# Kernel tuning notes

Measured on AMD Instinct MI355X. Metric: run time of the kernel, lower is better.

Reference implementation:

```python
import jax, jax.numpy as jnp
import numpy as np

B, T, C = 4, 2048, 2048  # batch, n_target, n_context
KEY_SIZE = 1024
VALUE_SIZE = 1024
NUM_HEADS = 16
KEY_HIDDEN = 64
HEAD_SIZE = VALUE_SIZE // NUM_HEADS  # 64
NORMALISE = True


def setup_inputs() -> dict:
    key = jax.random.key(0)
    ks = jax.random.split(key, 7)
    s = 0.02
    return {
        "queries": jax.random.normal(ks[0], (B, T, KEY_SIZE), jnp.float32),
        "keys": jax.random.normal(ks[1], (B, C, KEY_SIZE), jnp.float32),
        "values": jax.random.normal(ks[2], (B, C, VALUE_SIZE), jnp.float32),
        "Wq": jax.random.normal(ks[3], (NUM_HEADS * KEY_HIDDEN, KEY_SIZE), jnp.float32) * s,
        "Wk": jax.random.normal(ks[4], (NUM_HEADS * KEY_HIDDEN, KEY_SIZE), jnp.float32) * s,
        "Wv": jax.random.normal(ks[5], (NUM_HEADS * HEAD_SIZE, VALUE_SIZE), jnp.float32) * s,
        "Wo": jax.random.normal(ks[6], (VALUE_SIZE, NUM_HEADS * HEAD_SIZE), jnp.float32) * s,
    }


def reference(queries, keys, values, Wq, Wk, Wv, Wo):
    # Linear projections (torch nn.Linear: x @ W.T), reshape to heads
    q = (queries @ Wq.T).reshape(B, T, NUM_HEADS, KEY_HIDDEN)   # [B,T,H,Dk]
    k = (keys @ Wk.T).reshape(B, C, NUM_HEADS, KEY_HIDDEN)      # [B,C,H,Dk]
    v = (values @ Wv.T).reshape(B, C, NUM_HEADS, HEAD_SIZE)     # [B,C,H,Dv]
    scale = np.sqrt(KEY_HIDDEN).astype(np.float32)
    # Scores [B,H,T,C]
    scores = jnp.einsum('bthd,bchd->bhtc', q, k) / scale
    if NORMALISE:
        attn = jax.nn.softmax(scores, axis=-1)
    else:
        attn = jax.nn.sigmoid(scores)
    out = jnp.einsum('bhtc,bchd->bthd', attn, v)                # [B,T,H,Dv]
    out = out.reshape(B, T, NUM_HEADS * HEAD_SIZE)
    return out @ Wo.T                                            # [B,T,VALUE_SIZE]
```

## Files before the change

kernel.cpp:

```cpp
#include <hip/hip_runtime.h>
#include <stdint.h>

#define BATCH 4
#define SEQ   2048
#define EMB   1024
#define NH    16
#define HD    64

typedef __attribute__((ext_vector_type(4))) float  floatx4;
typedef __attribute__((ext_vector_type(8))) short  shortx8;

__device__ __forceinline__ unsigned short f2bf(float f) {
  unsigned u = __builtin_bit_cast(unsigned, f);
  u += 0x7FFFu + ((u >> 16) & 1u);
  return (unsigned short)(u >> 16);
}

__device__ __forceinline__ unsigned pack2bf(float a, float b) {
  return (unsigned)f2bf(a) | ((unsigned)f2bf(b) << 16);
}

__device__ __forceinline__ unsigned packtrunc(float a, float b) {
#if __has_builtin(__builtin_amdgcn_perm)
  return __builtin_amdgcn_perm(__builtin_bit_cast(unsigned, b),
                               __builtin_bit_cast(unsigned, a), 0x07060302u);
#else
  return (__builtin_bit_cast(unsigned, a) >> 16) |
         (__builtin_bit_cast(unsigned, b) & 0xFFFF0000u);
#endif
}

__device__ __forceinline__ float fexp2(float x) {
#if __has_builtin(__builtin_amdgcn_exp2f)
  return __builtin_amdgcn_exp2f(x);
#else
  return exp2f(x);
#endif
}

__device__ __forceinline__ void gl_lds16(const void* g, void* l) {
  __builtin_amdgcn_global_load_lds((const __attribute__((address_space(1))) void*)g,
                                   (__attribute__((address_space(3))) void*)l,
                                   16, 0, 0);
}

__device__ __forceinline__ void cast_body(const float* __restrict__ in,
                                          unsigned short* __restrict__ out, int bb, int t) {
  size_t i = (size_t)bb * 256 + t;
  const float4* p = (const float4*)in + i * 2;
  float4 f0 = p[0], f1 = p[1];
  uint4 o;
  o.x = pack2bf(f0.x, f0.y);
  o.y = pack2bf(f0.z, f0.w);
  o.z = pack2bf(f1.x, f1.y);
  o.w = pack2bf(f1.z, f1.w);
  ((uint4*)out)[i] = o;
}

__global__ __launch_bounds__(256) void cast_bf16(const float* __restrict__ in,
                                                 unsigned short* __restrict__ out) {
  cast_body(in, out, blockIdx.x, threadIdx.x);
}

__global__ __launch_bounds__(256) void cast_all(
    const float* __restrict__ q, const float* __restrict__ k, const float* __restrict__ v,
    const float* __restrict__ w0, const float* __restrict__ w1,
    const float* __restrict__ w2, const float* __restrict__ w3,
    unsigned short* __restrict__ oq, unsigned short* __restrict__ ok, unsigned short* __restrict__ ov,
    unsigned short* __restrict__ ow0, unsigned short* __restrict__ ow1,
    unsigned short* __restrict__ ow2, unsigned short* __restrict__ ow3) {
  int bb = blockIdx.x;
  const float* in; unsigned short* out;
  if      (bb < 4096)  { in = q;  out = oq; }
  else if (bb < 8192)  { in = k;  out = ok;  bb -= 4096; }
  else if (bb < 12288) { in = v;  out = ov;  bb -= 8192; }
  else if (bb < 12800) { in = w0; out = ow0; bb -= 12288; }
  else if (bb < 13312) { in = w1; out = ow1; bb -= 12800; }
  else if (bb < 13824) { in = w2; out = ow2; bb -= 13312; }
  else                 { in = w3; out = ow3; bb -= 13824; }
  cast_body(in, out, bb, threadIdx.x);
}

__global__ __launch_bounds__(256) void cast_w4(const float* __restrict__ i0, const float* __restrict__ i1,
                                               const float* __restrict__ i2, const float* __restrict__ i3,
                                               unsigned short* __restrict__ o0, unsigned short* __restrict__ o1,
                                               unsigned short* __restrict__ o2, unsigned short* __restrict__ o3) {
  int bb = blockIdx.x;
  const float* in; unsigned short* out;
  if      (bb < 512)  { in = i0; out = o0; }
  else if (bb < 1024) { in = i1; out = o1; bb -= 512; }
  else if (bb < 1536) { in = i2; out = o2; bb -= 1024; }
  else                { in = i3; out = o3; bb -= 1536; }
  cast_body(in, out, bb, threadIdx.x);
}

template <bool CF32>
__device__ __forceinline__ void gemm_body(const unsigned short* __restrict__ A,
                                          const unsigned short* __restrict__ Bt,
                                          void* __restrict__ Cp, float cscale) {
  constexpr int N = EMB, K = EMB;
  constexpr int BM = 128, BN = 128, BK = 64;
  __shared__ unsigned short As[BM * BK];
  __shared__ unsigned short Bs[BN * BK];
  const int t = threadIdx.x, w = t >> 6, lane = t & 63;
  const int quad = lane >> 4, lrow = lane & 15;
  const int m0 = blockIdx.y * BM, n0 = blockIdx.x * BN;
  const int wm = (w >> 1) * 64, wn = (w & 1) * 64;
  floatx4 acc[4][4] = {};

  const unsigned short* asrc[4];
  const unsigned short* bsrc[4];
#pragma unroll
  for (int i = 0; i < 4; i++) {
    int q = i * 256 + t;
    int r = q >> 3, kc = (q & 7) ^ (r & 7);
    asrc[i] = A + (size_t)(m0 + r) * K + kc * 8;
    bsrc[i] = Bt + (size_t)(n0 + r) * K + kc * 8;
  }

  for (int k0 = 0; k0 < K; k0 += BK) {
#pragma unroll
    for (int i = 0; i < 4; i++) {
      gl_lds16(asrc[i], (char*)As + (size_t)(i * 256 + w * 64) * 16);
      gl_lds16(bsrc[i], (char*)Bs + (size_t)(i * 256 + w * 64) * 16);
      asrc[i] += BK; bsrc[i] += BK;
    }
    __syncthreads();
#pragma unroll
    for (int ks = 0; ks < 2; ks++) {
      shortx8 a[4];
#pragma unroll
      for (int mi = 0; mi < 4; mi++) {
        int row = wm + mi * 16 + lrow;
        a[mi] = *(const shortx8*)(As + row * 64 + (((ks * 4 + quad) ^ (row & 7)) * 8));
      }
#pragma unroll
      for (int ni = 0; ni < 4; ni++) {
        int rowb = wn + ni * 16 + lrow;
        shortx8 b = *(const shortx8*)(Bs + rowb * 64 + (((ks * 4 + quad) ^ (rowb & 7)) * 8));
#pragma unroll
        for (int mi = 0; mi < 4; mi++)
          acc[mi][ni] = __builtin_amdgcn_mfma_f32_16x16x32_bf16(a[mi], b, acc[mi][ni], 0, 0, 0);
      }
    }
    __syncthreads();
  }
#pragma unroll
  for (int mi = 0; mi < 4; mi++)
#pragma unroll
    for (int ni = 0; ni < 4; ni++)
#pragma unroll
      for (int r = 0; r < 4; r++) {
        int row = m0 + wm + mi * 16 + quad * 4 + r;
        int col = n0 + wn + ni * 16 + lrow;
        float v = acc[mi][ni][r] * cscale;
        if constexpr (CF32) ((float*)Cp)[(size_t)row * N + col] = v;
        else                ((unsigned short*)Cp)[(size_t)row * N + col] = f2bf(v);
      }
}

__global__ __launch_bounds__(256, 2) void gemm_qkv(
    const unsigned short* __restrict__ Xq, const unsigned short* __restrict__ Xk,
    const unsigned short* __restrict__ Xv,
    const unsigned short* __restrict__ Wq, const unsigned short* __restrict__ Wk,
    const unsigned short* __restrict__ Wv,
    unsigned short* __restrict__ Oq, unsigned short* __restrict__ Ok,
    unsigned short* __restrict__ Ov, float sq) {
  const unsigned short *A, *Bt; unsigned short* C; float sc;
  if (blockIdx.z == 0)      { A = Xq; Bt = Wq; C = Oq; sc = sq; }
  else if (blockIdx.z == 1) { A = Xk; Bt = Wk; C = Ok; sc = 1.0f; }
  else                      { A = Xv; Bt = Wv; C = Ov; sc = 1.0f; }
  gemm_body<false>(A, Bt, C, sc);
}

__global__ __launch_bounds__(256, 2) void gemm_o(const unsigned short* __restrict__ A,
                                                 const unsigned short* __restrict__ Bt,
                                                 float* __restrict__ C) {
  gemm_body<true>(A, Bt, C, 1.0f);
}

__global__ __launch_bounds__(256) void transpose_v(const unsigned short* __restrict__ vp,
                                                   unsigned short* __restrict__ vT) {
  __shared__ unsigned short tile[64][72];
  const int c0 = blockIdx.x * 64, h = blockIdx.y, b = blockIdx.z;
  const int t = threadIdx.x;
#pragma unroll
  for (int i = 0; i < 2; i++) {
    int q = t + 256 * i;
    int r = q >> 3, dc = (q & 7) * 8;
    uint4 v = *(const uint4*)(vp + ((size_t)(b * SEQ + c0 + r)) * EMB + h * HD + dc);
    *(uint4*)&tile[r][dc] = v;
  }
  __syncthreads();
#pragma unroll
  for (int i = 0; i < 2; i++) {
    int q = t + 256 * i;
    int d = q >> 3, a = q & 7;
    unsigned e[8];
#pragma unroll
    for (int u = 0; u < 8; u++) {
      int cp = 8 * a + u;
      int c = 32 * (cp >> 5) + 16 * (cp & 1) + ((cp & 31) >> 1);
      e[u] = tile[c][d];
    }
    uint4 o;
    o.x = e[0] | (e[1] << 16); o.y = e[2] | (e[3] << 16);
    o.z = e[4] | (e[5] << 16); o.w = e[6] | (e[7] << 16);
    *(uint4*)(vT + ((size_t)((b * NH + h) * HD + d)) * SEQ + c0 + 8 * a) = o;
  }
}

__global__ __launch_bounds__(256, 3) void flash_attn(const unsigned short* __restrict__ qp,
                                                     const unsigned short* __restrict__ kp,
                                                     const unsigned short* __restrict__ vT,
                                                     unsigned short* __restrict__ ao) {
  __shared__ unsigned short Qs[128 * 64];
  __shared__ unsigned short Ks[2][64 * 64];
  __shared__ unsigned short Vts[2][64 * 64];
  __shared__ unsigned short Ps[4][16 * 40];
  const int t0 = blockIdx.x * 128, h = blockIdx.y, b = blockIdx.z;
  const int t = threadIdx.x, w = t >> 6, lane = t & 63;
  const int quad = lane >> 4, lrow = lane & 15;

#pragma unroll
  for (int i = 0; i < 4; i++) {
    int p = i * 256 + t;
    int r = p >> 3, kc = (p & 7) ^ (r & 7);
    gl_lds16(qp + ((size_t)(b * SEQ + t0 + r)) * EMB + h * HD + kc * 8,
             (char*)Qs + (size_t)(i * 256 + w * 64) * 16);
  }

  const unsigned short* ksrc[2];
  const unsigned short* vsrc[2];
#pragma unroll
  for (int i = 0; i < 2; i++) {
    int p = i * 256 + t;
    int r = p >> 3, kc = (p & 7) ^ (r & 7);
    ksrc[i] = kp + ((size_t)(b * SEQ + r)) * EMB + h * HD + kc * 8;
    vsrc[i] = vT + ((size_t)((b * NH + h) * HD + r)) * SEQ + kc * 8;
  }

#pragma unroll
  for (int i = 0; i < 2; i++) {
    gl_lds16(ksrc[i], (char*)Ks[0] + (size_t)(i * 256 + w * 64) * 16);
    gl_lds16(vsrc[i], (char*)Vts[0] + (size_t)(i * 256 + w * 64) * 16);
    ksrc[i] += 64 * EMB;
    vsrc[i] += 64;
  }

  float l_st[2][4] = {};
  floatx4 accO[2][4] = {};

  for (int it = 0; it < SEQ / 64; it++) {
    const int cur = it & 1;
    __syncthreads();
    if (it + 1 < SEQ / 64) {
#pragma unroll
      for (int i = 0; i < 2; i++) {
        gl_lds16(ksrc[i], (char*)Ks[cur ^ 1] + (size_t)(i * 256 + w * 64) * 16);
        gl_lds16(vsrc[i], (char*)Vts[cur ^ 1] + (size_t)(i * 256 + w * 64) * 16);
        ksrc[i] += 64 * EMB;
        vsrc[i] += 64;
      }
    }
    const unsigned short* Kc = Ks[cur];
    const unsigned short* Vc = Vts[cur];

    floatx4 accS[2][4] = {};
#pragma unroll
    for (int kk = 0; kk < 2; kk++) {
      int qk = quad + kk * 4;
      shortx8 afr[2];
#pragma unroll
      for (int mi = 0; mi < 2; mi++) {
        int row = w * 32 + mi * 16 + lrow;
        afr[mi] = *(const shortx8*)(Qs + row * 64 + ((qk ^ (row & 7)) * 8));
      }
#pragma unroll
      for (int ni = 0; ni < 4; ni++) {
        int rowb = ni * 16 + lrow;
        shortx8 bfr = *(const shortx8*)(Kc + rowb * 64 + ((qk ^ (rowb & 7)) * 8));
#pragma unroll
        for (int mi = 0; mi < 2; mi++)
          accS[mi][ni] = __builtin_amdgcn_mfma_f32_16x16x32_bf16(afr[mi], bfr, accS[mi][ni], 0, 0, 0);
      }
    }

#pragma unroll
    for (int hh = 0; hh < 2; hh++) {
      shortx8 pafr[2];
#pragma unroll
      for (int mi = 0; mi < 2; mi++) {
#pragma unroll
        for (int r = 0; r < 4; r++) {
          float p0 = fexp2(accS[mi][2 * hh][r]);
          float p1 = fexp2(accS[mi][2 * hh + 1][r]);
          l_st[mi][r] += p0 + p1;
          *(unsigned*)(&Ps[w][(quad * 4 + r) * 40 + lrow * 2]) = packtrunc(p0, p1);
        }
        pafr[mi] = *(const shortx8*)(&Ps[w][lrow * 40 + quad * 8]);
      }
#pragma unroll
      for (int nio = 0; nio < 4; nio++) {
        int d = nio * 16 + lrow;
        shortx8 bfr = *(const shortx8*)(Vc + d * 64 + ((((hh << 2) + quad) ^ (d & 7)) * 8));
#pragma unroll
        for (int mi = 0; mi < 2; mi++)
          accO[mi][nio] = __builtin_amdgcn_mfma_f32_16x16x32_bf16(pafr[mi], bfr, accO[mi][nio], 0, 0, 0);
      }
    }
  }

#pragma unroll
  for (int mi = 0; mi < 2; mi++)
#pragma unroll
    for (int r = 0; r < 4; r++) {
      float l = l_st[mi][r];
      l += __shfl_xor(l, 1);
      l += __shfl_xor(l, 2);
      l += __shfl_xor(l, 4);
      l += __shfl_xor(l, 8);
      float inv = 1.0f / l;
#pragma unroll
      for (int nio = 0; nio < 4; nio++) accO[mi][nio][r] *= inv;
    }
#pragma unroll
  for (int mi = 0; mi < 2; mi++)
#pragma unroll
    for (int nio = 0; nio < 4; nio++)
#pragma unroll
      for (int r = 0; r < 4; r++) {
        int row = t0 + w * 32 + mi * 16 + quad * 4 + r;
        int col = h * HD + nio * 16 + lrow;
        ao[((size_t)(b * SEQ + row)) * EMB + col] = f2bf(accO[mi][nio][r]);
      }
}

extern "C" void kernel_launch(void* const* d_in, const int* in_sizes, int n_in,
                              void* d_out, int out_size, void* d_ws, size_t ws_size,
                              hipStream_t stream) {
  const float* queries = (const float*)d_in[0];
  const float* keys    = (const float*)d_in[1];
  const float* values  = (const float*)d_in[2];
  const float* Wq      = (const float*)d_in[3];
  const float* Wk      = (const float*)d_in[4];
  const float* Wv      = (const float*)d_in[5];
  const float* Wo      = (const float*)d_in[6];

  char* ws = (char*)d_ws;
  const size_t MB = 1ull << 20;
  const float SC2 = 0.125f * 1.44269504088896341f;

  unsigned short* wq_b = (unsigned short*)(ws + 0 * MB);
  unsigned short* wk_b = (unsigned short*)(ws + 2 * MB);
  unsigned short* wv_b = (unsigned short*)(ws + 4 * MB);
  unsigned short* wo_b = (unsigned short*)(ws + 6 * MB);

  dim3 gg(EMB / 128, (BATCH * SEQ) / 128);

  if (ws_size >= 104 * MB) {
    unsigned short* Xq = (unsigned short*)(ws + 8 * MB);
    unsigned short* Xk = (unsigned short*)(ws + 24 * MB);
    unsigned short* Xv = (unsigned short*)(ws + 40 * MB);
    unsigned short* qp = (unsigned short*)(ws + 56 * MB);
    unsigned short* kp = (unsigned short*)(ws + 72 * MB);
    unsigned short* vp = (unsigned short*)(ws + 88 * MB);
    unsigned short* vT = Xk;
    unsigned short* ao = Xq;

    cast_all<<<14336, 256, 0, stream>>>(queries, keys, values, Wq, Wk, Wv, Wo,
                                        Xq, Xk, Xv, wq_b, wk_b, wv_b, wo_b);
    gemm_qkv<<<dim3(gg.x, gg.y, 3), 256, 0, stream>>>(Xq, Xk, Xv, wq_b, wk_b, wv_b,
                                                      qp, kp, vp, SC2);
    transpose_v<<<dim3(SEQ / 64, NH, BATCH), 256, 0, stream>>>(vp, vT);
    flash_attn<<<dim3(SEQ / 128, NH, BATCH), 256, 0, stream>>>(qp, kp, vT, ao);
    gemm_o<<<gg, 256, 0, stream>>>(ao, wo_b, (float*)d_out);
  } else {
    unsigned short* X  = (unsigned short*)(ws + 8 * MB);
    unsigned short* qp = (unsigned short*)(ws + 24 * MB);
    unsigned short* kp = (unsigned short*)(ws + 40 * MB);
    unsigned short* vp = (unsigned short*)(ws + 56 * MB);
    unsigned short* vT = (unsigned short*)(ws + 72 * MB);
    unsigned short* ao = X;

    cast_w4<<<2048, 256, 0, stream>>>(Wq, Wk, Wv, Wo, wq_b, wk_b, wv_b, wo_b);
    cast_bf16<<<4096, 256, 0, stream>>>(queries, X);
    gemm_qkv<<<dim3(gg.x, gg.y, 1), 256, 0, stream>>>(X, X, X, wq_b, wq_b, wq_b,
                                                      qp, qp, qp, SC2);
    cast_bf16<<<4096, 256, 0, stream>>>(keys, X);
    gemm_qkv<<<dim3(gg.x, gg.y, 1), 256, 0, stream>>>(X, X, X, wk_b, wk_b, wk_b,
                                                      kp, kp, kp, 1.0f);
    cast_bf16<<<4096, 256, 0, stream>>>(values, X);
    gemm_qkv<<<dim3(gg.x, gg.y, 1), 256, 0, stream>>>(X, X, X, wv_b, wv_b, wv_b,
                                                      vp, vp, vp, 1.0f);
    transpose_v<<<dim3(SEQ / 64, NH, BATCH), 256, 0, stream>>>(vp, vT);
    flash_attn<<<dim3(SEQ / 128, NH, BATCH), 256, 0, stream>>>(qp, kp, vT, ao);
    gemm_o<<<gg, 256, 0, stream>>>(ao, wo_b, (float*)d_out);
  }
}
```

Before: 349.7 us.

## Fuse V transpose into QKV GEMM epilogue and single-buffer flash attention tiles

The V projection GEMM now writes its output already transposed into the head-major vT layout through an LDS staging tile, so the separate transpose_v kernel and its round trip through global memory go away. Flash attention drops its K/V double buffering in favour of a single buffer with a sync on each side of the load, and raises its launch bound to 4 blocks per CU. The gemm_qkv kernel now reserves an extra ~34KB LDS transpose tile on every block (even the Q/K ones), which may lower GEMM occupancy. The attention loop also loses the overlap between loading the next tile and computing the current one, and relies on higher occupancy to hide that latency instead.

```diff
diff --git a/kernel.cpp b/kernel.cpp
--- a/kernel.cpp
+++ b/kernel.cpp
@@ -94,14 +94,15 @@
   cast_body(in, out, bb, threadIdx.x);
 }
 
-template <bool CF32>
+#define TST 136
+template <int MODE>
 __device__ __forceinline__ void gemm_body(const unsigned short* __restrict__ A,
                                           const unsigned short* __restrict__ Bt,
-                                          void* __restrict__ Cp, float cscale) {
+                                          void* __restrict__ Cp, float cscale,
+                                          unsigned short* As, unsigned short* Bs,
+                                          unsigned short* Ts) {
   constexpr int N = EMB, K = EMB;
   constexpr int BM = 128, BN = 128, BK = 64;
-  __shared__ unsigned short As[BM * BK];
-  __shared__ unsigned short Bs[BN * BK];
   const int t = threadIdx.x, w = t >> 6, lane = t & 63;
   const int quad = lane >> 4, lrow = lane & 15;
   const int m0 = blockIdx.y * BM, n0 = blockIdx.x * BN;
@@ -145,18 +146,46 @@
     }
     __syncthreads();
   }
-#pragma unroll
-  for (int mi = 0; mi < 4; mi++)
-#pragma unroll
-    for (int ni = 0; ni < 4; ni++)
-#pragma unroll
-      for (int r = 0; r < 4; r++) {
-        int row = m0 + wm + mi * 16 + quad * 4 + r;
-        int col = n0 + wn + ni * 16 + lrow;
-        float v = acc[mi][ni][r] * cscale;
-        if constexpr (CF32) ((float*)Cp)[(size_t)row * N + col] = v;
-        else                ((unsigned short*)Cp)[(size_t)row * N + col] = f2bf(v);
-      }
+
+  if constexpr (MODE == 2) {
+#pragma unroll
+    for (int u = 0; u < 2; u++)
+#pragma unroll
+      for (int ni = 0; ni < 4; ni++) {
+        uint4 p;
+        p.x = pack2bf(acc[2 * u][ni][0], acc[2 * u + 1][ni][0]);
+        p.y = pack2bf(acc[2 * u][ni][1], acc[2 * u + 1][ni][1]);
+        p.z = pack2bf(acc[2 * u][ni][2], acc[2 * u + 1][ni][2]);
+        p.w = pack2bf(acc[2 * u][ni][3], acc[2 * u + 1][ni][3]);
+        int col = wn + ni * 16 + lrow;
+        int cloc = wm + u * 32 + quad * 8;
+        *(uint4*)(Ts + col * TST + cloc) = p;
+      }
+    __syncthreads();
+    unsigned short* vTout = (unsigned short*)Cp;
+    const int b = m0 >> 11, cbase = m0 & 2047, h0 = n0 >> 6;
+#pragma unroll
+    for (int i = 0; i < 8; i++) {
+      int g = t + 256 * i;
+      int hh2 = g >> 10, d = (g >> 4) & 63, a = g & 15;
+      uint4 v = *(const uint4*)(Ts + (hh2 * 64 + d) * TST + a * 8);
+      *(uint4*)(vTout + ((size_t)((b * NH + h0 + hh2) * HD + d)) * SEQ + cbase + a * 8) = v;
+    }
+    __syncthreads();
+  } else {
+#pragma unroll
+    for (int mi = 0; mi < 4; mi++)
+#pragma unroll
+      for (int ni = 0; ni < 4; ni++)
+#pragma unroll
+        for (int r = 0; r < 4; r++) {
+          int row = m0 + wm + mi * 16 + quad * 4 + r;
+          int col = n0 + wn + ni * 16 + lrow;
+          float v = acc[mi][ni][r] * cscale;
+          if constexpr (MODE == 1) ((float*)Cp)[(size_t)row * N + col] = v;
+          else                     ((unsigned short*)Cp)[(size_t)row * N + col] = f2bf(v);
+        }
+  }
 }
 
 __global__ __launch_bounds__(256, 2) void gemm_qkv(
@@ -165,58 +194,45 @@
     const unsigned short* __restrict__ Wq, const unsigned short* __restrict__ Wk,
     const unsigned short* __restrict__ Wv,
     unsigned short* __restrict__ Oq, unsigned short* __restrict__ Ok,
-    unsigned short* __restrict__ Ov, float sq) {
-  const unsigned short *A, *Bt; unsigned short* C; float sc;
-  if (blockIdx.z == 0)      { A = Xq; Bt = Wq; C = Oq; sc = sq; }
-  else if (blockIdx.z == 1) { A = Xk; Bt = Wk; C = Ok; sc = 1.0f; }
-  else                      { A = Xv; Bt = Wv; C = Ov; sc = 1.0f; }
-  gemm_body<false>(A, Bt, C, sc);
-}
-
+    unsigned short* __restrict__ OvT, float sq) {
+  __shared__ unsigned short As[128 * 64];
+  __shared__ unsigned short Bs[128 * 64];
+  __shared__ unsigned short Ts[128 * TST];
+  if (blockIdx.z == 0)      gemm_body<0>(Xq, Wq, Oq, sq,   As, Bs, Ts);
+  else if (blockIdx.z == 1) gemm_body<0>(Xk, Wk, Ok, 1.0f, As, Bs, Ts);
+  else                      gemm_body<2>(Xv, Wv, OvT, 1.0f, As, Bs, Ts);
+}
+
+__global__ __launch_bounds__(256, 2) void gemm_b(const unsigned short* __restrict__ A,
+                                                 const unsigned short* __restrict__ Bt,
+                                                 unsigned short* __restrict__ C, float sc) {
+  __shared__ unsigned short As[128 * 64];
+  __shared__ unsigned short Bs[128 * 64];
+  gemm_body<0>(A, Bt, C, sc, As, Bs, nullptr);
+}
+__global__ __launch_bounds__(256, 2) void gemm_vt(const unsigned short* __restrict__ A,
+                                                  const unsigned short* __restrict__ Bt,
+                                                  unsigned short* __restrict__ C) {
+  __shared__ unsigned short As[128 * 64];
+  __shared__ unsigned short Bs[128 * 64];
+  __shared__ unsigned short Ts[128 * TST];
+  gemm_body<2>(A, Bt, C, 1.0f, As, Bs, Ts);
+}
 __global__ __launch_bounds__(256, 2) void gemm_o(const unsigned short* __restrict__ A,
                                                  const unsigned short* __restrict__ Bt,
                                                  float* __restrict__ C) {
-  gemm_body<true>(A, Bt, C, 1.0f);
-}
-
-__global__ __launch_bounds__(256) void transpose_v(const unsigned short* __restrict__ vp,
-                                                   unsigned short* __restrict__ vT) {
-  __shared__ unsigned short tile[64][72];
-  const int c0 = blockIdx.x * 64, h = blockIdx.y, b = blockIdx.z;
-  const int t = threadIdx.x;
-#pragma unroll
-  for (int i = 0; i < 2; i++) {
-    int q = t + 256 * i;
-    int r = q >> 3, dc = (q & 7) * 8;
-    uint4 v = *(const uint4*)(vp + ((size_t)(b * SEQ + c0 + r)) * EMB + h * HD + dc);
-    *(uint4*)&tile[r][dc] = v;
-  }
-  __syncthreads();
-#pragma unroll
-  for (int i = 0; i < 2; i++) {
-    int q = t + 256 * i;
-    int d = q >> 3, a = q & 7;
-    unsigned e[8];
-#pragma unroll
-    for (int u = 0; u < 8; u++) {
-      int cp = 8 * a + u;
-      int c = 32 * (cp >> 5) + 16 * (cp & 1) + ((cp & 31) >> 1);
-      e[u] = tile[c][d];
-    }
-    uint4 o;
-    o.x = e[0] | (e[1] << 16); o.y = e[2] | (e[3] << 16);
-    o.z = e[4] | (e[5] << 16); o.w = e[6] | (e[7] << 16);
-    *(uint4*)(vT + ((size_t)((b * NH + h) * HD + d)) * SEQ + c0 + 8 * a) = o;
-  }
-}
-
-__global__ __launch_bounds__(256, 3) void flash_attn(const unsigned short* __restrict__ qp,
+  __shared__ unsigned short As[128 * 64];
+  __shared__ unsigned short Bs[128 * 64];
+  gemm_body<1>(A, Bt, C, 1.0f, As, Bs, nullptr);
+}
+
+__global__ __launch_bounds__(256, 4) void flash_attn(const unsigned short* __restrict__ qp,
                                                      const unsigned short* __restrict__ kp,
                                                      const unsigned short* __restrict__ vT,
                                                      unsigned short* __restrict__ ao) {
   __shared__ unsigned short Qs[128 * 64];
-  __shared__ unsigned short Ks[2][64 * 64];
-  __shared__ unsigned short Vts[2][64 * 64];
+  __shared__ unsigned short Ks[64 * 64];
+  __shared__ unsigned short Vts[64 * 64];
   __shared__ unsigned short Ps[4][16 * 40];
   const int t0 = blockIdx.x * 128, h = blockIdx.y, b = blockIdx.z;
   const int t = threadIdx.x, w = t >> 6, lane = t & 63;
@@ -240,31 +256,19 @@
     vsrc[i] = vT + ((size_t)((b * NH + h) * HD + r)) * SEQ + kc * 8;
   }
 
-#pragma unroll
-  for (int i = 0; i < 2; i++) {
-    gl_lds16(ksrc[i], (char*)Ks[0] + (size_t)(i * 256 + w * 64) * 16);
-    gl_lds16(vsrc[i], (char*)Vts[0] + (size_t)(i * 256 + w * 64) * 16);
-    ksrc[i] += 64 * EMB;
-    vsrc[i] += 64;
-  }
-
   float l_st[2][4] = {};
   floatx4 accO[2][4] = {};
 
-  for (int it = 0; it < SEQ / 64; it++) {
-    const int cur = it & 1;
-    __syncthreads();
-    if (it + 1 < SEQ / 64) {
-#pragma unroll
-      for (int i = 0; i < 2; i++) {
-        gl_lds16(ksrc[i], (char*)Ks[cur ^ 1] + (size_t)(i * 256 + w * 64) * 16);
-        gl_lds16(vsrc[i], (char*)Vts[cur ^ 1] + (size_t)(i * 256 + w * 64) * 16);
-        ksrc[i] += 64 * EMB;
-        vsrc[i] += 64;
-      }
-    }
-    const unsigned short* Kc = Ks[cur];
-    const unsigned short* Vc = Vts[cur];
+  for (int c0 = 0; c0 < SEQ; c0 += 64) {
+    __syncthreads();
+#pragma unroll
+    for (int i = 0; i < 2; i++) {
+      gl_lds16(ksrc[i], (char*)Ks + (size_t)(i * 256 + w * 64) * 16);
+      gl_lds16(vsrc[i], (char*)Vts + (size_t)(i * 256 + w * 64) * 16);
+      ksrc[i] += 64 * EMB;
+      vsrc[i] += 64;
+    }
+    __syncthreads();
 
     floatx4 accS[2][4] = {};
 #pragma unroll
@@ -279,7 +283,7 @@
 #pragma unroll
       for (int ni = 0; ni < 4; ni++) {
         int rowb = ni * 16 + lrow;
-        shortx8 bfr = *(const shortx8*)(Kc + rowb * 64 + ((qk ^ (rowb & 7)) * 8));
+        shortx8 bfr = *(const shortx8*)(Ks + rowb * 64 + ((qk ^ (rowb & 7)) * 8));
 #pragma unroll
         for (int mi = 0; mi < 2; mi++)
           accS[mi][ni] = __builtin_amdgcn_mfma_f32_16x16x32_bf16(afr[mi], bfr, accS[mi][ni], 0, 0, 0);
@@ -303,7 +307,7 @@
 #pragma unroll
       for (int nio = 0; nio < 4; nio++) {
         int d = nio * 16 + lrow;
-        shortx8 bfr = *(const shortx8*)(Vc + d * 64 + ((((hh << 2) + quad) ^ (d & 7)) * 8));
+        shortx8 bfr = *(const shortx8*)(Vts + d * 64 + ((((hh << 2) + quad) ^ (d & 7)) * 8));
 #pragma unroll
         for (int mi = 0; mi < 2; mi++)
           accO[mi][nio] = __builtin_amdgcn_mfma_f32_16x16x32_bf16(pafr[mi], bfr, accO[mi][nio], 0, 0, 0);
@@ -364,36 +368,29 @@
     unsigned short* Xv = (unsigned short*)(ws + 40 * MB);
     unsigned short* qp = (unsigned short*)(ws + 56 * MB);
     unsigned short* kp = (unsigned short*)(ws + 72 * MB);
-    unsigned short* vp = (unsigned short*)(ws + 88 * MB);
-    unsigned short* vT = Xk;
+    unsigned short* vT = (unsigned short*)(ws + 88 * MB);
     unsigned short* ao = Xq;
 
     cast_all<<<14336, 256, 0, stream>>>(queries, keys, values, Wq, Wk, Wv, Wo,
                                         Xq, Xk, Xv, wq_b, wk_b, wv_b, wo_b);
     gemm_qkv<<<dim3(gg.x, gg.y, 3), 256, 0, stream>>>(Xq, Xk, Xv, wq_b, wk_b, wv_b,
-                                                      qp, kp, vp, SC2);
-    transpose_v<<<dim3(SEQ / 64, NH, BATCH), 256, 0, stream>>>(vp, vT);
+                                                      qp, kp, vT, SC2);
     flash_attn<<<dim3(SEQ / 128, NH, BATCH), 256, 0, stream>>>(qp, kp, vT, ao);
     gemm_o<<<gg, 256, 0, stream>>>(ao, wo_b, (float*)d_out);
   } else {
     unsigned short* X  = (unsigned short*)(ws + 8 * MB);
     unsigned short* qp = (unsigned short*)(ws + 24 * MB);
     unsigned short* kp = (unsigned short*)(ws + 40 * MB);
-    unsigned short* vp = (unsigned short*)(ws + 56 * MB);
-    unsigned short* vT = (unsigned short*)(ws + 72 * MB);
+    unsigned short* vT = (unsigned short*)(ws + 56 * MB);
     unsigned short* ao = X;
 
     cast_w4<<<2048, 256, 0, stream>>>(Wq, Wk, Wv, Wo, wq_b, wk_b, wv_b, wo_b);
     cast_bf16<<<4096, 256, 0, stream>>>(queries, X);
-    gemm_qkv<<<dim3(gg.x, gg.y, 1), 256, 0, stream>>>(X, X, X, wq_b, wq_b, wq_b,
-                                                      qp, qp, qp, SC2);
+    gemm_b<<<gg, 256, 0, stream>>>(X, wq_b, qp, SC2);
     cast_bf16<<<4096, 256, 0, stream>>>(keys, X);
-    gemm_qkv<<<dim3(gg.x, gg.y, 1), 256, 0, stream>>>(X, X, X, wk_b, wk_b, wk_b,
-                                                      kp, kp, kp, 1.0f);
+    gemm_b<<<gg, 256, 0, stream>>>(X, wk_b, kp, 1.0f);
     cast_bf16<<<4096, 256, 0, stream>>>(values, X);
-    gemm_qkv<<<dim3(gg.x, gg.y, 1), 256, 0, stream>>>(X, X, X, wv_b, wv_b, wv_b,
-                                                      vp, vp, vp, 1.0f);
-    transpose_v<<<dim3(SEQ / 64, NH, BATCH), 256, 0, stream>>>(vp, vT);
+    gemm_vt<<<gg, 256, 0, stream>>>(X, wv_b, vT);
     flash_attn<<<dim3(SEQ / 128, NH, BATCH), 256, 0, stream>>>(qp, kp, vT, ao);
     gemm_o<<<gg, 256, 0, stream>>>(ao, wo_b, (float*)d_out);
   }
```

After: 327.3 us. 1.07x faster.
